# Performance work log

Measured on AMD Instinct MI355X. Metric: run time of the kernel, lower is better.

Reference implementation:

```python
import jax, jax.numpy as jnp
import numpy as np

MARGIN = 1.0

def _pairwise_sqdist(z):
    # ||zi - zj||^2 = ||zi||^2 + ||zj||^2 - 2 zi.zj
    sq = jnp.sum(z * z, axis=-1)  # [N]
    d2 = sq[:, None] + sq[None, :] - 2.0 * (z @ z.T)
    return jnp.maximum(d2, 0.0)

def _safe_sqrt(d2):
    # sqrt with well-defined gradient at 0 (matches cdist values; diag = 0)
    pos = d2 > 0.0
    return jnp.where(pos, jnp.sqrt(jnp.where(pos, d2, 1.0)), 0.0)

def setup_inputs() -> dict:
    key = jax.random.key(0)
    k1, k2 = jax.random.split(key)
    z = jax.random.normal(k1, (8192, 128), dtype=jnp.float32)
    labels = jax.random.randint(k2, (8192,), 0, 100, dtype=jnp.int64)
    return {"z": z, "labels": labels}

def reference(z, labels):
    d2 = _pairwise_sqdist(z)              # [N, N] squared distances
    dist = _safe_sqrt(d2)                 # [N, N] distances
    label_eq = labels[:, None] == labels[None, :]
    pos = jnp.where(label_eq, d2, 0.0)
    neg = jnp.where(label_eq, 0.0, jnp.square(jax.nn.relu(MARGIN - dist)))
    return jnp.mean(pos + neg)
```

## Files before the change

### kernel.cpp

```cpp
#include <hip/hip_runtime.h>
#include <stdint.h>


#define NROWS 8192
#define DIMK  128
#define NB    64
#define NPERS 512

typedef __attribute__((ext_vector_type(4))) float f32x4;

__global__ __launch_bounds__(256) void prep_kernel(
    const float* __restrict__ z, unsigned char* __restrict__ zb,
    float* __restrict__ sq) {
  int tid = threadIdx.x;
  int row = (blockIdx.x << 3) + (tid >> 5);
  int c32 = tid & 31;
  float4 x = ((const float4*)(z + (size_t)row * DIMK))[c32];
  int u = __builtin_amdgcn_cvt_pk_fp8_f32(x.x, x.y, 0, false);
  u     = __builtin_amdgcn_cvt_pk_fp8_f32(x.z, x.w, u, true);
  float r0 = __builtin_amdgcn_cvt_f32_fp8(u, 0);
  float r1 = __builtin_amdgcn_cvt_f32_fp8(u, 1);
  float r2 = __builtin_amdgcn_cvt_f32_fp8(u, 2);
  float r3 = __builtin_amdgcn_cvt_f32_fp8(u, 3);
  float s = (r0 * r0 + r1 * r1) + (r2 * r2 + r3 * r3);
  int k0 = c32 << 2;
  int g  = (((k0 >> 3) & 3) << 2) | (k0 >> 5);
  int p  = ((g ^ (row & 15)) << 3) + (k0 & 7);
  *(uint32_t*)(zb + (size_t)row * DIMK + p) = (uint32_t)u;
  #pragma unroll
  for (int off = 16; off; off >>= 1) s += __shfl_down(s, off, 32);
  if (c32 == 0) sq[row] = s;
}

__device__ __forceinline__ void decode_tile_x(int x, int n, int& bi, int& bj) {
  int rem = n, k = 0, len = NB - x;
  while (rem >= len) { rem -= len; ++k; len -= 8; }
  bi = x + (k << 3);
  bj = bi + rem;
}

__global__ __launch_bounds__(512, 4) void loss_kernel(
    const unsigned char* __restrict__ zb, const float* __restrict__ sq,
    const int* __restrict__ labels, float* __restrict__ out) {
  __shared__ float red[8];

  int tid = threadIdx.x, lane = tid & 63, wave = tid >> 6;
  int wm = wave >> 1, wn = wave & 1;
  int lc = lane & 15;
  int q  = lane >> 4;

  float psum_acc = 0.f;

  int x = blockIdx.x & 7;
  int s = blockIdx.x >> 3;
  int tcount = 288 - 8 * x;

  int rA0 = ((wm << 5)      + lc) * 128;
  int rA1 = ((wm << 5) + 16 + lc) * 128;
  int rB0 = ((wn << 6)      + lc) * 128;
  int rB1 = ((wn << 6) + 16 + lc) * 128;
  int rB2 = ((wn << 6) + 32 + lc) * 128;
  int rB3 = ((wn << 6) + 48 + lc) * 128;

  for (int n = s; n < tcount; n += 64) {
    int bi, bj;
    decode_tile_x(x, n, bi, bj);
    const unsigned char* Ab = zb + (((size_t)bi << 7) * DIMK);
    const unsigned char* Bb = zb + (((size_t)bj << 7) * DIMK);

    f32x4 acc[2][4] = {};
    #pragma unroll
    for (int ks = 0; ks < 4; ++ks) {
      int so = ((((q << 2) | ks) ^ lc) << 3);
      long a0 = *(const long*)(Ab + rA0 + so);
      long a1 = *(const long*)(Ab + rA1 + so);
      long b0 = *(const long*)(Bb + rB0 + so);
      long b1 = *(const long*)(Bb + rB1 + so);
      long b2 = *(const long*)(Bb + rB2 + so);
      long b3 = *(const long*)(Bb + rB3 + so);
      acc[0][0] = __builtin_amdgcn_mfma_f32_16x16x32_fp8_fp8(a0, b0, acc[0][0], 0, 0, 0);
      acc[0][1] = __builtin_amdgcn_mfma_f32_16x16x32_fp8_fp8(a0, b1, acc[0][1], 0, 0, 0);
      acc[0][2] = __builtin_amdgcn_mfma_f32_16x16x32_fp8_fp8(a0, b2, acc[0][2], 0, 0, 0);
      acc[0][3] = __builtin_amdgcn_mfma_f32_16x16x32_fp8_fp8(a0, b3, acc[0][3], 0, 0, 0);
      acc[1][0] = __builtin_amdgcn_mfma_f32_16x16x32_fp8_fp8(a1, b0, acc[1][0], 0, 0, 0);
      acc[1][1] = __builtin_amdgcn_mfma_f32_16x16x32_fp8_fp8(a1, b1, acc[1][1], 0, 0, 0);
      acc[1][2] = __builtin_amdgcn_mfma_f32_16x16x32_fp8_fp8(a1, b2, acc[1][2], 0, 0, 0);
      acc[1][3] = __builtin_amdgcn_mfma_f32_16x16x32_fp8_fp8(a1, b3, acc[1][3], 0, 0, 0);
    }

    const float* sqA = sq     + ((size_t)bi << 7);
    const int*   laA = labels + ((size_t)bi << 7);
    const float* sqB = sq     + ((size_t)bj << 7);
    const int*   laB = labels + ((size_t)bj << 7);

    int r0 = q << 2;
    float sn_[4]; int ln_[4];
    #pragma unroll
    for (int j = 0; j < 4; ++j) {
      int nidx = (wn << 6) + (j << 4) + lc;
      sn_[j] = sqB[nidx]; ln_[j] = laB[nidx];
    }
    float ps0 = 0.f, ps1 = 0.f, ps2 = 0.f, ps3 = 0.f;
    float mnall = 1e30f;
    #pragma unroll
    for (int i = 0; i < 2; ++i) {
      int mb = (wm << 5) + (i << 4) + r0;
      f32x4 sm4 = *(const f32x4*)&sqA[mb];
      int4  lm4 = *(const int4*)&laA[mb];
      #pragma unroll
      for (int j = 0; j < 4; ++j) {
        float d0  = fmaf(-2.f, acc[i][j][0], sm4[0] + sn_[j]);
        float d1  = fmaf(-2.f, acc[i][j][1], sm4[1] + sn_[j]);
        float d2_ = fmaf(-2.f, acc[i][j][2], sm4[2] + sn_[j]);
        float d3  = fmaf(-2.f, acc[i][j][3], sm4[3] + sn_[j]);
        mnall = fminf(mnall, fminf(fminf(d0, d1), fminf(d2_, d3)));
        ps0 += (lm4.x == ln_[j]) ? d0  : 0.f;
        ps1 += (lm4.y == ln_[j]) ? d1  : 0.f;
        ps2 += (lm4.z == ln_[j]) ? d2_ : 0.f;
        ps3 += (lm4.w == ln_[j]) ? d3  : 0.f;
      }
    }
    if (__builtin_expect(__any(mnall < 1.f), 0)) {
      ps0 = ps1 = ps2 = ps3 = 0.f;
      #pragma unroll
      for (int i = 0; i < 2; ++i) {
        int mb = (wm << 5) + (i << 4) + r0;
        f32x4 sm4 = *(const f32x4*)&sqA[mb];
        int4  lm4 = *(const int4*)&laA[mb];
        #pragma unroll
        for (int j = 0; j < 4; ++j) {
          float dc, tt;
          dc = fmaxf(fmaf(-2.f, acc[i][j][0], sm4[0] + sn_[j]), 0.f);
          tt = fmaxf(1.f - sqrtf(dc), 0.f);
          ps0 += (lm4.x == ln_[j]) ? dc : tt * tt;
          dc = fmaxf(fmaf(-2.f, acc[i][j][1], sm4[1] + sn_[j]), 0.f);
          tt = fmaxf(1.f - sqrtf(dc), 0.f);
          ps1 += (lm4.y == ln_[j]) ? dc : tt * tt;
          dc = fmaxf(fmaf(-2.f, acc[i][j][2], sm4[2] + sn_[j]), 0.f);
          tt = fmaxf(1.f - sqrtf(dc), 0.f);
          ps2 += (lm4.z == ln_[j]) ? dc : tt * tt;
          dc = fmaxf(fmaf(-2.f, acc[i][j][3], sm4[3] + sn_[j]), 0.f);
          tt = fmaxf(1.f - sqrtf(dc), 0.f);
          ps3 += (lm4.w == ln_[j]) ? dc : tt * tt;
        }
      }
    }
    float w = (bi == bj) ? 1.f : 2.f;
    psum_acc += w * ((ps0 + ps1) + (ps2 + ps3));
  }

  psum_acc *= (1.f / (8192.f * 8192.f));
  #pragma unroll
  for (int off = 32; off; off >>= 1) psum_acc += __shfl_down(psum_acc, off);
  if (lane == 0) red[wave] = psum_acc;
  __syncthreads();
  if (tid == 0) {
    float sum = 0.f;
    #pragma unroll
    for (int k = 0; k < 8; ++k) sum += red[k];
    atomicAdd(out, sum);
  }
}

extern "C" void kernel_launch(void* const* d_in, const int* in_sizes, int n_in,
                              void* d_out, int out_size, void* d_ws, size_t ws_size,
                              hipStream_t stream) {
  const float* z      = (const float*)d_in[0];
  const int*   labels = (const int*)d_in[1];
  float*       out    = (float*)d_out;
  unsigned char* zb   = (unsigned char*)d_ws;
  float* sq           = (float*)((char*)d_ws + (size_t)NROWS * DIMK);

  prep_kernel<<<NROWS / 8, 256, 0, stream>>>(z, zb, sq);
  loss_kernel<<<NPERS, 512, 0, stream>>>(zb, sq, labels, out);
}
```

Measured before the change: 82.88 us.

## Stage tiles into LDS with triple-buffered async global_load_lds pipeline

Loss tiles are now copied into shared memory with direct global-to-LDS loads, three tiles in flight, with explicit vmcnt waits and barriers. The same is done for the per-tile squared norms and labels. This replaces redundant per-wave global loads of A/B fragments and hides memory latency behind MFMA work. The grid is halved (256 blocks, occupancy hint 2) to pay for the ~100KB of LDS per block, which reduces parallelism and depends on hand-counted vmcnt values staying correct.

```diff
diff --git a/kernel.cpp b/kernel.cpp
--- a/kernel.cpp
+++ b/kernel.cpp
@@ -5,9 +5,13 @@
 #define NROWS 8192
 #define DIMK  128
 #define NB    64
-#define NPERS 512
+#define NPERS 256
+#define TSTRIDE 32
 
 typedef __attribute__((ext_vector_type(4))) float f32x4;
+
+#define AS_GLOBAL __attribute__((address_space(1)))
+#define AS_LDS    __attribute__((address_space(3)))
 
 __global__ __launch_bounds__(256) void prep_kernel(
     const float* __restrict__ z, unsigned char* __restrict__ zb,
@@ -39,9 +43,11 @@
   bj = bi + rem;
 }
 
-__global__ __launch_bounds__(512, 4) void loss_kernel(
+__global__ __launch_bounds__(512, 2) void loss_kernel(
     const unsigned char* __restrict__ zb, const float* __restrict__ sq,
     const int* __restrict__ labels, float* __restrict__ out) {
+  __shared__ __align__(16) unsigned char buf[3][32768];
+  __shared__ __align__(16) unsigned char sqlab[3][2048];
   __shared__ float red[8];
 
   int tid = threadIdx.x, lane = tid & 63, wave = tid >> 6;
@@ -49,35 +55,75 @@
   int lc = lane & 15;
   int q  = lane >> 4;
 
+  int sl_isB  = wave >> 2;
+  int sl_isLa = (wave >> 1) & 1;
+  int sl_half = wave & 1;
+
   float psum_acc = 0.f;
 
   int x = blockIdx.x & 7;
   int s = blockIdx.x >> 3;
   int tcount = 288 - 8 * x;
 
-  int rA0 = ((wm << 5)      + lc) * 128;
-  int rA1 = ((wm << 5) + 16 + lc) * 128;
-  int rB0 = ((wn << 6)      + lc) * 128;
-  int rB1 = ((wn << 6) + 16 + lc) * 128;
-  int rB2 = ((wn << 6) + 32 + lc) * 128;
-  int rB3 = ((wn << 6) + 48 + lc) * 128;
-
-  for (int n = s; n < tcount; n += 64) {
+  #define STAGE(ti, bf) do {                                                 \
+    int tbi, tbj; decode_tile_x(x, (ti), tbi, tbj);                          \
+    const unsigned char* Ab_ = zb + (((size_t)tbi << 7) * DIMK);             \
+    const unsigned char* Bb_ = zb + (((size_t)tbj << 7) * DIMK);             \
+    _Pragma("unroll")                                                        \
+    for (int it = 0; it < 2; ++it) {                                         \
+      int L0 = (it << 9) + (wave << 6);                                      \
+      __builtin_amdgcn_global_load_lds(                                      \
+          (const AS_GLOBAL void*)(uintptr_t)(Ab_ + (size_t)(L0 + lane) * 16),\
+          (AS_LDS void*)(uintptr_t)(&buf[(bf)][(size_t)L0 * 16]), 16, 0, 0); \
+      __builtin_amdgcn_global_load_lds(                                      \
+          (const AS_GLOBAL void*)(uintptr_t)(Bb_ + (size_t)(L0 + lane) * 16),\
+          (AS_LDS void*)(uintptr_t)(&buf[(bf)][16384 + (size_t)L0 * 16]),    \
+          16, 0, 0);                                                         \
+    }                                                                        \
+    const char* p0_ = sl_isLa ? (const char*)labels : (const char*)sq;       \
+    const char* src_ = p0_ + ((size_t)((sl_isB ? tbj : tbi) << 7) << 2)      \
+                           + (sl_half << 8);                                 \
+    if (lane < 16)                                                           \
+      __builtin_amdgcn_global_load_lds(                                      \
+          (const AS_GLOBAL void*)(uintptr_t)(src_ + lane * 16),              \
+          (AS_LDS void*)(uintptr_t)(&sqlab[(bf)][wave << 8]), 16, 0, 0);     \
+  } while (0)
+
+  int inflight = 0;
+  #pragma unroll
+  for (int p = 0; p < 3; ++p) {
+    int np = s + p * TSTRIDE;
+    if (np < tcount) { STAGE(np, p); ++inflight; }
+  }
+
+  int cur = 0;
+  for (int n = s;; n += TSTRIDE) {
+    if (inflight >= 3)      asm volatile("s_waitcnt vmcnt(10)" ::: "memory");
+    else if (inflight == 2) asm volatile("s_waitcnt vmcnt(5)"  ::: "memory");
+    else                    asm volatile("s_waitcnt vmcnt(0)"  ::: "memory");
+    asm volatile("s_barrier" ::: "memory");
+    __builtin_amdgcn_sched_barrier(0);
+
     int bi, bj;
     decode_tile_x(x, n, bi, bj);
-    const unsigned char* Ab = zb + (((size_t)bi << 7) * DIMK);
-    const unsigned char* Bb = zb + (((size_t)bj << 7) * DIMK);
+
+    const unsigned char* ldsA = &buf[cur][0];
+    const unsigned char* ldsB = &buf[cur][16384];
+    const float* sqAl = (const float*)&sqlab[cur][0];
+    const int*   laAl = (const int*)&sqlab[cur][512];
+    const float* sqBl = (const float*)&sqlab[cur][1024];
+    const int*   laBl = (const int*)&sqlab[cur][1536];
 
     f32x4 acc[2][4] = {};
     #pragma unroll
     for (int ks = 0; ks < 4; ++ks) {
       int so = ((((q << 2) | ks) ^ lc) << 3);
-      long a0 = *(const long*)(Ab + rA0 + so);
-      long a1 = *(const long*)(Ab + rA1 + so);
-      long b0 = *(const long*)(Bb + rB0 + so);
-      long b1 = *(const long*)(Bb + rB1 + so);
-      long b2 = *(const long*)(Bb + rB2 + so);
-      long b3 = *(const long*)(Bb + rB3 + so);
+      long a0 = *(const long*)(ldsA + ((wm << 5)      + lc) * 128 + so);
+      long a1 = *(const long*)(ldsA + ((wm << 5) + 16 + lc) * 128 + so);
+      long b0 = *(const long*)(ldsB + ((wn << 6)      + lc) * 128 + so);
+      long b1 = *(const long*)(ldsB + ((wn << 6) + 16 + lc) * 128 + so);
+      long b2 = *(const long*)(ldsB + ((wn << 6) + 32 + lc) * 128 + so);
+      long b3 = *(const long*)(ldsB + ((wn << 6) + 48 + lc) * 128 + so);
       acc[0][0] = __builtin_amdgcn_mfma_f32_16x16x32_fp8_fp8(a0, b0, acc[0][0], 0, 0, 0);
       acc[0][1] = __builtin_amdgcn_mfma_f32_16x16x32_fp8_fp8(a0, b1, acc[0][1], 0, 0, 0);
       acc[0][2] = __builtin_amdgcn_mfma_f32_16x16x32_fp8_fp8(a0, b2, acc[0][2], 0, 0, 0);
@@ -88,25 +134,20 @@
       acc[1][3] = __builtin_amdgcn_mfma_f32_16x16x32_fp8_fp8(a1, b3, acc[1][3], 0, 0, 0);
     }
 
-    const float* sqA = sq     + ((size_t)bi << 7);
-    const int*   laA = labels + ((size_t)bi << 7);
-    const float* sqB = sq     + ((size_t)bj << 7);
-    const int*   laB = labels + ((size_t)bj << 7);
-
     int r0 = q << 2;
     float sn_[4]; int ln_[4];
     #pragma unroll
     for (int j = 0; j < 4; ++j) {
       int nidx = (wn << 6) + (j << 4) + lc;
-      sn_[j] = sqB[nidx]; ln_[j] = laB[nidx];
+      sn_[j] = sqBl[nidx]; ln_[j] = laBl[nidx];
     }
     float ps0 = 0.f, ps1 = 0.f, ps2 = 0.f, ps3 = 0.f;
     float mnall = 1e30f;
     #pragma unroll
     for (int i = 0; i < 2; ++i) {
       int mb = (wm << 5) + (i << 4) + r0;
-      f32x4 sm4 = *(const f32x4*)&sqA[mb];
-      int4  lm4 = *(const int4*)&laA[mb];
+      f32x4 sm4 = *(const f32x4*)&sqAl[mb];
+      int4  lm4 = *(const int4*)&laAl[mb];
       #pragma unroll
       for (int j = 0; j < 4; ++j) {
         float d0  = fmaf(-2.f, acc[i][j][0], sm4[0] + sn_[j]);
@@ -125,8 +166,8 @@
       #pragma unroll
       for (int i = 0; i < 2; ++i) {
         int mb = (wm << 5) + (i << 4) + r0;
-        f32x4 sm4 = *(const f32x4*)&sqA[mb];
-        int4  lm4 = *(const int4*)&laA[mb];
+        f32x4 sm4 = *(const f32x4*)&sqAl[mb];
+        int4  lm4 = *(const int4*)&laAl[mb];
         #pragma unroll
         for (int j = 0; j < 4; ++j) {
           float dc, tt;
@@ -147,6 +188,16 @@
     }
     float w = (bi == bj) ? 1.f : 2.f;
     psum_acc += w * ((ps0 + ps1) + (ps2 + ps3));
+    --inflight;
+
+    bool hasNext = (n + TSTRIDE) < tcount;
+    if (!hasNext) break;
+
+    __builtin_amdgcn_sched_barrier(0);
+    asm volatile("s_barrier" ::: "memory");
+    int np = n + 3 * TSTRIDE;
+    if (np < tcount) { STAGE(np, cur); ++inflight; }
+    cur = (cur == 2) ? 0 : cur + 1;
   }
 
   psum_acc *= (1.f / (8192.f * 8192.f));
```

Result: faster. 77.32 us (-6.7%).
